# Kernel tuning notes

Hardware: AMD Instinct MI355X
Metric: run time of the kernel (lower is better)

The kernel has to match this reference:

```python
import jax, jax.numpy as jnp
import numpy as np

ALPHA, BETA, THRESH, T = 0.9, 0.8, 1.0, 10


def _heaviside(x):
    return (x > 0).astype(x.dtype)


def _conv(x, w, b, stride):
    y = jax.lax.conv_general_dilated(
        x, w, window_strides=(stride, stride), padding='VALID',
        dimension_numbers=('NCHW', 'OIHW', 'NCHW'))
    return jax.nn.relu(y + b[None, :, None, None])


def setup_inputs() -> dict:
    key = jax.random.key(0)
    ks = jax.random.split(key, 16)
    B = 128
    state = jax.random.uniform(ks[0], (B, 3, 224, 224), dtype=jnp.float32)
    history = jax.random.uniform(ks[1], (B, 90), dtype=jnp.float32)
    fc_in = 64 * 24 * 24 + 90  # 36954

    def w(k, shape, fan_in):
        return jax.random.normal(k, shape, dtype=jnp.float32) * (1.0 / np.sqrt(fan_in))

    return {
        'state': state, 'history': history,
        'cw1': w(ks[2], (32, 3, 8, 8), 3 * 8 * 8), 'cb1': jnp.zeros((32,), jnp.float32),
        'cw2': w(ks[3], (64, 32, 4, 4), 32 * 4 * 4), 'cb2': jnp.zeros((64,), jnp.float32),
        'cw3': w(ks[4], (64, 64, 3, 3), 64 * 3 * 3), 'cb3': jnp.zeros((64,), jnp.float32),
        'w1': w(ks[5], (128, fc_in), fc_in), 'b1': jnp.zeros((128,), jnp.float32),
        'w2': w(ks[6], (256, 128), 128), 'b2': jnp.zeros((256,), jnp.float32),
        'w3': w(ks[7], (9, 256), 256), 'b3': jnp.zeros((9,), jnp.float32),
    }


def reference(state, history, cw1, cb1, cw2, cb2, cw3, cb3, w1, b1, w2, b2, w3, b3):
    B = state.shape[0]
    f = _conv(state, cw1, cb1, 4)
    f = _conv(f, cw2, cb2, 2)
    f = _conv(f, cw3, cb3, 1)
    x = jnp.concatenate([f.reshape(B, -1), history], axis=1)  # (B, 36954)
    # encoding='constant' -> input (hence h1) is identical every timestep
    h1 = x @ w1.T + b1  # (B,128)

    def lif(h, mem, syn):
        new_syn = ALPHA * syn + h
        new_mem = BETA * mem + new_syn
        out = _heaviside(new_mem - THRESH)
        return out, new_mem - out * THRESH, new_syn

    z = lambda d: jnp.zeros((B, d), x.dtype)
    carry0 = (z(128), z(128), z(256), z(256), z(9), z(9), z(9))

    def step(carry, _):
        mem1, syn1, mem2, syn2, mem3, syn3, pot = carry
        spk1, mem1, syn1 = lif(h1, mem1, syn1)
        h2 = spk1 @ w2.T + b2
        spk2, mem2, syn2 = lif(h2, mem2, syn2)
        h3 = spk2 @ w3.T + b3
        syn3 = ALPHA * syn3 + h3
        mem3 = BETA * mem3 + syn3
        pot = pot + mem3
        return (mem1, syn1, mem2, syn2, mem3, syn3, pot), None

    carry, _ = jax.lax.scan(step, carry0, None, length=T)
    return carry[6] / T
```

## Files before the change

### kernel.cpp

```cpp
#include <hip/hip_runtime.h>

#define ALPHA 0.9f
#define BETA  0.8f
#define XS 36960

typedef _Float16 f16;
typedef _Float16 f16x8 __attribute__((ext_vector_type(8)));
typedef float f32x4 __attribute__((ext_vector_type(4)));
typedef unsigned int u32;

struct F4 { float x, y, z, w; };

#define GLOAD_LDS16(gsrc, ldst)                                        \
  __builtin_amdgcn_global_load_lds(                                    \
      (const __attribute__((address_space(1))) void*)(gsrc),           \
      (__attribute__((address_space(3))) void*)(ldst), 16, 0, 0)

__device__ inline u32 hpair(u32 d0, u32 d1) {
#if __has_builtin(__builtin_amdgcn_perm)
  return __builtin_amdgcn_perm(d1, d0, 0x05040100u);
#else
  return (d0 & 0xffffu) | (d1 << 16);
#endif
}
__device__ inline u32 lpair(u32 d0, u32 d1) {
#if __has_builtin(__builtin_amdgcn_perm)
  return __builtin_amdgcn_perm(d1, d0, 0x07060302u);
#else
  return (d0 >> 16) | (d1 & 0xffff0000u);
#endif
}

__device__ inline u32 pack_hl(float v) {
  f16 h = (f16)v;
  f16 l = (f16)(v - (float)h);
  return (u32)__builtin_bit_cast(unsigned short, h) |
         ((u32)__builtin_bit_cast(unsigned short, l) << 16);
}


__global__ __launch_bounds__(256) void prep_weights_kernel(
    const float* __restrict__ cw1, const float* __restrict__ cw2,
    const float* __restrict__ cw3, const float* __restrict__ w2,
    f16* __restrict__ w1h, f16* __restrict__ w1l,
    f16* __restrict__ w2h, f16* __restrict__ w2l,
    f16* __restrict__ w3h, f16* __restrict__ w3l,
    float* __restrict__ w2q) {
  int i = blockIdx.x * 256 + threadIdx.x;
  if (i < 6144)  { float v = cw1[i]; f16 h = (f16)v; w1h[i] = h; w1l[i] = (f16)(v - (float)h); }
  if (i < 32768) { float v = cw2[i]; f16 h = (f16)v; w2h[i] = h; w2l[i] = (f16)(v - (float)h); }
  if (i < 49152) {
    int oc = i / 768, r = i % 768;
    int c = r / 12, rr = r % 12, kh = rr >> 2, kw = rr & 3;
    float v = (kw < 3) ? cw3[oc * 576 + c * 9 + kh * 3 + kw] : 0.f;
    f16 h = (f16)v; w3h[i] = h; w3l[i] = (f16)(v - (float)h);
  }
  if (i < 32768) {
    int j = i >> 7, k = i & 127;
    w2q[((k >> 2) * 256 + j) * 4 + (k & 3)] = w2[i];
  }
}

__global__ __launch_bounds__(512) void conv1_kernel(
    const float* __restrict__ in, const f16* __restrict__ wh,
    const f16* __restrict__ wl, const float* __restrict__ bias,
    u32* __restrict__ out) {
  constexpr int K = 192, KCH = 6, OW = 55, OHW = 3025, NPB = 256;
  __shared__ __attribute__((aligned(16))) f16 Ah[2 * 512], Al[2 * 512];
  __shared__ __attribute__((aligned(16))) float Bf[16 * 512];

  const int n = blockIdx.y, pos0 = blockIdx.x * NPB;
  const int t = threadIdx.x;
  const int w = t >> 6, lane = t & 63, quad = lane >> 4, l16 = lane & 15;
  const float* __restrict__ inb = in + (size_t)n * 3 * 224 * 224;

  const int rq = (t >> 4) & 3;
  int base[2];
#pragma unroll
  for (int si = 0; si < 2; ++si) {
    int s = t + si * 512;
    int pos = pos0 + (s >> 6) * 16 + (s & 15);
    if (pos > OHW - 1) pos = OHW - 1;
    int oh = pos / OW, ow = pos - oh * OW;
    base[si] = oh * 4 * 224 + ow * 4;
  }
  const int am = (t >> 6) * 16 + (t & 15);
  const int ak = ((t >> 4) & 3) * 8;

  int posv[2];
#pragma unroll
  for (int ntl = 0; ntl < 2; ++ntl)
    posv[ntl] = pos0 + (w * 2 + ntl) * 16 + l16;

  f32x4 acc[2][2] = {};

  for (int kt = 0; kt < KCH; ++kt) {
    __syncthreads();
    if (t < 128) {
      *(f16x8*)&Ah[t * 8] = *(const f16x8*)&wh[am * K + kt * 32 + ak];
      *(f16x8*)&Al[t * 8] = *(const f16x8*)&wl[am * K + kt * 32 + ak];
    }
    {
      int r = kt * 4 + rq;
      int c = r >> 3, kh = r & 7;
      int rowoff = c * 50176 + kh * 224;
#pragma unroll
      for (int si = 0; si < 2; ++si)
#pragma unroll
        for (int half = 0; half < 2; ++half)
          GLOAD_LDS16(inb + rowoff + base[si] + half * 4,
                      &Bf[(si * 8 + w) * 512 + half * 256]);
    }
    __syncthreads();

    f16x8 ah0 = *(const f16x8*)&Ah[0 * 512 + lane * 8];
    f16x8 ah1 = *(const f16x8*)&Ah[1 * 512 + lane * 8];
    f16x8 al0 = *(const f16x8*)&Al[0 * 512 + lane * 8];
    f16x8 al1 = *(const f16x8*)&Al[1 * 512 + lane * 8];
    f16x8 bh[2], bl[2];
#pragma unroll
    for (int ntl = 0; ntl < 2; ++ntl) {
      const float* bp = &Bf[(w * 2 + ntl) * 512 + lane * 4];
      float4 v0 = *(const float4*)bp;
      float4 v1 = *(const float4*)(bp + 256);
      float vv[8] = {v0.x, v0.y, v0.z, v0.w, v1.x, v1.y, v1.z, v1.w};
#pragma unroll
      for (int e = 0; e < 8; ++e) {
        f16 h = (f16)vv[e];
        bh[ntl][e] = h;
        bl[ntl][e] = (f16)(vv[e] - (float)h);
      }
    }
    acc[0][0] = __builtin_amdgcn_mfma_f32_16x16x32_f16(ah0, bh[0], acc[0][0], 0, 0, 0);
    acc[0][0] = __builtin_amdgcn_mfma_f32_16x16x32_f16(ah0, bl[0], acc[0][0], 0, 0, 0);
    acc[0][0] = __builtin_amdgcn_mfma_f32_16x16x32_f16(al0, bh[0], acc[0][0], 0, 0, 0);
    acc[1][0] = __builtin_amdgcn_mfma_f32_16x16x32_f16(ah1, bh[0], acc[1][0], 0, 0, 0);
    acc[1][0] = __builtin_amdgcn_mfma_f32_16x16x32_f16(ah1, bl[0], acc[1][0], 0, 0, 0);
    acc[1][0] = __builtin_amdgcn_mfma_f32_16x16x32_f16(al1, bh[0], acc[1][0], 0, 0, 0);
    acc[0][1] = __builtin_amdgcn_mfma_f32_16x16x32_f16(ah0, bh[1], acc[0][1], 0, 0, 0);
    acc[0][1] = __builtin_amdgcn_mfma_f32_16x16x32_f16(ah0, bl[1], acc[0][1], 0, 0, 0);
    acc[0][1] = __builtin_amdgcn_mfma_f32_16x16x32_f16(al0, bh[1], acc[0][1], 0, 0, 0);
    acc[1][1] = __builtin_amdgcn_mfma_f32_16x16x32_f16(ah1, bh[1], acc[1][1], 0, 0, 0);
    acc[1][1] = __builtin_amdgcn_mfma_f32_16x16x32_f16(ah1, bl[1], acc[1][1], 0, 0, 0);
    acc[1][1] = __builtin_amdgcn_mfma_f32_16x16x32_f16(al1, bh[1], acc[1][1], 0, 0, 0);
  }

#pragma unroll
  for (int mtl = 0; mtl < 2; ++mtl)
#pragma unroll
    for (int ntl = 0; ntl < 2; ++ntl)
#pragma unroll
      for (int r = 0; r < 4; ++r) {
        int oc  = mtl * 16 + quad * 4 + r;
        int pos = posv[ntl];
        if (pos < OHW) {
          float v = acc[mtl][ntl][r] + bias[oc];
          v = v > 0.f ? v : 0.f;
          out[((size_t)n * 32 + oc) * OHW + pos] = pack_hl(v);
        }
      }
}

template<int IC, int KH, int KWP, int KWV, int S, int IH, int IW,
         int OW, int OHW, int OC, int NPB, bool OUT_X>
__global__ __launch_bounds__(NPB * 4) void convhl_kernel(
    const u32* __restrict__ in, const f16* __restrict__ wh,
    const f16* __restrict__ wl, const float* __restrict__ bias,
    void* __restrict__ outv) {
  constexpr int K = IC * KH * KWP;
  constexpr int KCH = K / 32;
  constexpr int BS = NPB * 4;
  __shared__ __attribute__((aligned(16))) f16 Ah[4 * 512], Al[4 * 512];
  __shared__ __attribute__((aligned(16))) u32 Bhl[2][BS * 4];

  const int n = blockIdx.y, pos0 = blockIdx.x * NPB;
  const int t = threadIdx.x;
  const int w = t >> 6, lane = t & 63, quad = lane >> 4, l16 = lane & 15;
  const int woc = w & 1, wpos = w >> 1;
  const u32* __restrict__ inb = in + (size_t)n * IC * IH * IW;

  int pos = pos0 + (t >> 6) * 16 + (t & 15);
  if (pos > OHW - 1) pos = OHW - 1;
  int oh = pos / OW, ow = pos - oh * OW;
  const int ohS = oh * S, owS = ow * S;
  const int rq = ((t >> 4) & 3) * 2;
  const int am = (t >> 6) * 16 + (t & 15);
  const int ak = ((t >> 4) & 3) * 8;

  int posv[2];
#pragma unroll
  for (int ntl = 0; ntl < 2; ++ntl)
    posv[ntl] = pos0 + (wpos * 2 + ntl) * 16 + l16;

  f32x4 acc[2][2] = {};

  for (int kt = 0; kt < KCH; ++kt) {
    __syncthreads();
    if (t < 256) {
      *(f16x8*)&Ah[t * 8] = *(const f16x8*)&wh[am * K + kt * 32 + ak];
      *(f16x8*)&Al[t * 8] = *(const f16x8*)&wl[am * K + kt * 32 + ak];
    }
#pragma unroll
    for (int half = 0; half < 2; ++half) {
      int row = kt * 8 + rq + half;
      int c = row / KH, kh = row - c * KH;
      const u32* p = inb + ((size_t)c * IH + ohS + kh) * IW + owS;
      uint4 d;
      d.x = p[0]; d.y = p[1]; d.z = p[2];
      d.w = (KWV < KWP) ? 0u : p[3];
      *(uint4*)&Bhl[half][t * 4] = d;
    }
    __syncthreads();

    f16x8 ah0 = *(const f16x8*)&Ah[(woc * 2 + 0) * 512 + lane * 8];
    f16x8 ah1 = *(const f16x8*)&Ah[(woc * 2 + 1) * 512 + lane * 8];
    f16x8 al0 = *(const f16x8*)&Al[(woc * 2 + 0) * 512 + lane * 8];
    f16x8 al1 = *(const f16x8*)&Al[(woc * 2 + 1) * 512 + lane * 8];
    f16x8 bh[2], bl[2];
#pragma unroll
    for (int ntl = 0; ntl < 2; ++ntl) {
      int sl = ((wpos * 2 + ntl) * 64 + lane) * 4;
      uint4 q0 = *(const uint4*)&Bhl[0][sl];
      uint4 q1 = *(const uint4*)&Bhl[1][sl];
      uint4 hv, lv;
      hv.x = hpair(q0.x, q0.y); lv.x = lpair(q0.x, q0.y);
      hv.y = hpair(q0.z, q0.w); lv.y = lpair(q0.z, q0.w);
      hv.z = hpair(q1.x, q1.y); lv.z = lpair(q1.x, q1.y);
      hv.w = hpair(q1.z, q1.w); lv.w = lpair(q1.z, q1.w);
      bh[ntl] = __builtin_bit_cast(f16x8, hv);
      bl[ntl] = __builtin_bit_cast(f16x8, lv);
    }
    acc[0][0] = __builtin_amdgcn_mfma_f32_16x16x32_f16(ah0, bh[0], acc[0][0], 0, 0, 0);
    acc[0][0] = __builtin_amdgcn_mfma_f32_16x16x32_f16(ah0, bl[0], acc[0][0], 0, 0, 0);
    acc[0][0] = __builtin_amdgcn_mfma_f32_16x16x32_f16(al0, bh[0], acc[0][0], 0, 0, 0);
    acc[1][0] = __builtin_amdgcn_mfma_f32_16x16x32_f16(ah1, bh[0], acc[1][0], 0, 0, 0);
    acc[1][0] = __builtin_amdgcn_mfma_f32_16x16x32_f16(ah1, bl[0], acc[1][0], 0, 0, 0);
    acc[1][0] = __builtin_amdgcn_mfma_f32_16x16x32_f16(al1, bh[0], acc[1][0], 0, 0, 0);
    acc[0][1] = __builtin_amdgcn_mfma_f32_16x16x32_f16(ah0, bh[1], acc[0][1], 0, 0, 0);
    acc[0][1] = __builtin_amdgcn_mfma_f32_16x16x32_f16(ah0, bl[1], acc[0][1], 0, 0, 0);
    acc[0][1] = __builtin_amdgcn_mfma_f32_16x16x32_f16(al0, bh[1], acc[0][1], 0, 0, 0);
    acc[1][1] = __builtin_amdgcn_mfma_f32_16x16x32_f16(ah1, bh[1], acc[1][1], 0, 0, 0);
    acc[1][1] = __builtin_amdgcn_mfma_f32_16x16x32_f16(ah1, bl[1], acc[1][1], 0, 0, 0);
    acc[1][1] = __builtin_amdgcn_mfma_f32_16x16x32_f16(al1, bh[1], acc[1][1], 0, 0, 0);
  }

#pragma unroll
  for (int mtl = 0; mtl < 2; ++mtl)
#pragma unroll
    for (int ntl = 0; ntl < 2; ++ntl)
#pragma unroll
      for (int r = 0; r < 4; ++r) {
        int oc = (woc * 2 + mtl) * 16 + quad * 4 + r;
        int p2 = posv[ntl];
        if (p2 < OHW) {
          float v = acc[mtl][ntl][r] + bias[oc];
          v = v > 0.f ? v : 0.f;
          if constexpr (OUT_X)
            ((float*)outv)[(size_t)n * XS + oc * OHW + p2] = v;
          else
            ((u32*)outv)[((size_t)n * OC + oc) * OHW + p2] = pack_hl(v);
        }
      }
}

__global__ __launch_bounds__(256) void histpack_kernel(
    const float* __restrict__ h, float* __restrict__ x) {
  int i = blockIdx.x * 256 + threadIdx.x;
  if (i < 128 * 96) {
    int n = i / 96, k = i % 96;
    x[(size_t)n * XS + 36864 + k] = (k < 90) ? h[n * 90 + k] : 0.f;
  }
}

#define FC1_KT 289
__global__ __launch_bounds__(256) void fc1_kernel(
    const float* __restrict__ x, const float* __restrict__ w1,
    float* __restrict__ P) {
  int kt = blockIdx.x >> 2;
  int b4 = blockIdx.x & 3;
  int t  = threadIdx.x;
  int bq = t & 3, jq = t >> 2;
  __shared__ float xs[32 * 36];
  __shared__ float wsm[128 * 36];
  float acc[8][2];
#pragma unroll
  for (int bb = 0; bb < 8; ++bb)
#pragma unroll
    for (int jj = 0; jj < 2; ++jj) acc[bb][jj] = 0.f;

  int cs = t & 7;
  int rs = t >> 3;
#pragma unroll 1
  for (int s = 0; s < 4; ++s) {
    int k0 = kt * 128 + s * 32;
    int gk = k0 + cs * 4;
    __syncthreads();
    {
      float4 xv;
      if (gk < 36954)
        xv = *(const float4*)&x[(size_t)(b4 * 32 + rs) * XS + gk];
      else
        xv = make_float4(0.f, 0.f, 0.f, 0.f);
      *(float4*)&xs[rs * 36 + cs * 4] = xv;
    }
#pragma unroll
    for (int p = 0; p < 4; ++p) {
      int r = rs + p * 32;
      float4 wv;
      if (gk + 4 <= 36954) {
        F4 u = *(const F4*)&w1[(size_t)r * 36954 + gk];
        wv = make_float4(u.x, u.y, u.z, u.w);
      } else if (gk < 36954) {
        wv.x = w1[(size_t)r * 36954 + gk];
        wv.y = (gk + 1 < 36954) ? w1[(size_t)r * 36954 + gk + 1] : 0.f;
        wv.z = 0.f; wv.w = 0.f;
      } else {
        wv = make_float4(0.f, 0.f, 0.f, 0.f);
      }
      *(float4*)&wsm[r * 36 + cs * 4] = wv;
    }
    __syncthreads();
#pragma unroll 1
    for (int kk = 0; kk < 32; kk += 4) {
      float4 xv[8], wv[2];
#pragma unroll
      for (int i = 0; i < 8; ++i)
        xv[i] = *(const float4*)&xs[(bq + 4 * i) * 36 + kk];
#pragma unroll
      for (int i = 0; i < 2; ++i)
        wv[i] = *(const float4*)&wsm[(jq + 64 * i) * 36 + kk];
#pragma unroll
      for (int bb = 0; bb < 8; ++bb)
#pragma unroll
        for (int jj = 0; jj < 2; ++jj) {
          acc[bb][jj] = fmaf(xv[bb].x, wv[jj].x, acc[bb][jj]);
          acc[bb][jj] = fmaf(xv[bb].y, wv[jj].y, acc[bb][jj]);
          acc[bb][jj] = fmaf(xv[bb].z, wv[jj].z, acc[bb][jj]);
          acc[bb][jj] = fmaf(xv[bb].w, wv[jj].w, acc[bb][jj]);
        }
    }
  }
  float* Pb = P + (size_t)kt * 16384;
#pragma unroll
  for (int bb = 0; bb < 8; ++bb)
#pragma unroll
    for (int jj = 0; jj < 2; ++jj)
      Pb[(b4 * 32 + bq + 4 * bb) * 128 + jq + 64 * jj] = acc[bb][jj];
}

__global__ __launch_bounds__(64) void reduce_p_kernel(
    const float* __restrict__ P, const float* __restrict__ b1,
    float* __restrict__ h1s) {
  int idx = blockIdx.x * 64 + threadIdx.x;
  int j = idx & 127;
  float a0 = 0.f, a1 = 0.f, a2 = 0.f, a3 = 0.f;
  int kt = 0;
  for (; kt + 31 < FC1_KT; kt += 32) {
    float v[32];
#pragma unroll
    for (int q = 0; q < 32; ++q)
      v[q] = P[(size_t)(kt + q) * 16384 + idx];
#pragma unroll
    for (int q = 0; q < 32; q += 4) {
      a0 += v[q]; a1 += v[q + 1]; a2 += v[q + 2]; a3 += v[q + 3];
    }
  }
  for (; kt + 3 < FC1_KT; kt += 4) {
    a0 += P[(size_t)(kt + 0) * 16384 + idx];
    a1 += P[(size_t)(kt + 1) * 16384 + idx];
    a2 += P[(size_t)(kt + 2) * 16384 + idx];
    a3 += P[(size_t)(kt + 3) * 16384 + idx];
  }
  for (; kt < FC1_KT; ++kt) a0 += P[(size_t)kt * 16384 + idx];
  h1s[idx] = ((a0 + a1) + (a2 + a3)) + b1[j];
}

__global__ __launch_bounds__(256, 1) void recur_kernel(
    const float* __restrict__ h1s,
    const float4* __restrict__ w2q,
    const float* __restrict__ b2,
    const float* __restrict__ w3,
    const float* __restrict__ b3,
    float* __restrict__ out) {
  int b = blockIdx.x;
  int t = threadIdx.x;
  __shared__ float spk1s[128];
  __shared__ float spk2s[256];
  __shared__ float w3s[9 * 256];
  __shared__ float part[9][16];
  float4 w2c[32];
#pragma unroll
  for (int k4 = 0; k4 < 32; ++k4) w2c[k4] = w2q[k4 * 256 + t];
  for (int i = t; i < 9 * 256; i += 256) w3s[i] = w3[i];
  float h1 = (t < 128) ? h1s[b * 128 + t] : 0.f;
  float mem1 = 0.f, syn1 = 0.f, mem2 = 0.f, syn2 = 0.f;
  float b2v = b2[t];
  float mem3 = 0.f, syn3 = 0.f, pot = 0.f;
  float b3v = (t < 9) ? b3[t] : 0.f;
  int j3 = t >> 4, p = t & 15;
  __syncthreads();

  for (int step = 0; step < 10; ++step) {
    if (t < 128) {
      syn1 = ALPHA * syn1 + h1;
      mem1 = BETA * mem1 + syn1;
      float s = (mem1 > 1.0f) ? 1.0f : 0.0f;
      mem1 -= s;
      spk1s[t] = s;
    }
    __syncthreads();
    float h2 = b2v;
#pragma unroll
    for (int k4 = 0; k4 < 32; ++k4) {
      float4 s = *(const float4*)&spk1s[k4 * 4];
      h2 = fmaf(s.x, w2c[k4].x, h2);
      h2 = fmaf(s.y, w2c[k4].y, h2);
      h2 = fmaf(s.z, w2c[k4].z, h2);
      h2 = fmaf(s.w, w2c[k4].w, h2);
    }
    syn2 = ALPHA * syn2 + h2;
    mem2 = BETA * mem2 + syn2;
    float s2 = (mem2 > 1.0f) ? 1.0f : 0.0f;
    mem2 -= s2;
    spk2s[t] = s2;
    __syncthreads();
    if (t < 144) {
      float a = 0.f;
      const float* wr = &w3s[j3 * 256 + p * 16];
      const float* sp = &spk2s[p * 16];
#pragma unroll
      for (int e = 0; e < 16; ++e) a = fmaf(sp[e], wr[e], a);
      part[j3][p] = a;
    }
    __syncthreads();
    if (t < 9) {
      float a = b3v;
#pragma unroll
      for (int p2 = 0; p2 < 16; ++p2) a += part[t][p2];
      syn3 = ALPHA * syn3 + a;
      mem3 = BETA * mem3 + syn3;
      pot += mem3;
    }
  }
  if (t < 9) out[b * 9 + t] = pot * 0.1f;
}

extern "C" void kernel_launch(void* const* d_in, const int* in_sizes, int n_in,
                              void* d_out, int out_size, void* d_ws, size_t ws_size,
                              hipStream_t stream) {
  const float* state   = (const float*)d_in[0];
  const float* history = (const float*)d_in[1];
  const float* cw1 = (const float*)d_in[2];
  const float* cb1 = (const float*)d_in[3];
  const float* cw2 = (const float*)d_in[4];
  const float* cb2 = (const float*)d_in[5];
  const float* cw3 = (const float*)d_in[6];
  const float* cb3 = (const float*)d_in[7];
  const float* w1  = (const float*)d_in[8];
  const float* b1  = (const float*)d_in[9];
  const float* w2  = (const float*)d_in[10];
  const float* b2  = (const float*)d_in[11];
  const float* w3  = (const float*)d_in[12];
  const float* b3  = (const float*)d_in[13];
  float* out = (float*)d_out;
  char* ws = (char*)d_ws;

  u32*   f1hl = (u32*)(ws + 0);
  float* xb   = (float*)(ws + 0);
  u32*   f2hl = (u32*)(ws + 49561600);
  float* P    = (float*)(ws + 49561600);
  f16* wf1h = (f16*)(ws + 71712768);
  f16* wf1l = (f16*)(ws + 71725056);
  f16* wf2h = (f16*)(ws + 71737344);
  f16* wf2l = (f16*)(ws + 71802880);
  f16* wf3h = (f16*)(ws + 71868416);
  f16* wf3l = (f16*)(ws + 71966720);
  float* w2q = (float*)(ws + 72065024);
  float* h1s = (float*)(ws + 72196096);

  prep_weights_kernel<<<192, 256, 0, stream>>>(cw1, cw2, cw3, w2,
                                               wf1h, wf1l, wf2h, wf2l,
                                               wf3h, wf3l, w2q);
  conv1_kernel<<<dim3(12, 128), 512, 0, stream>>>(state, wf1h, wf1l, cb1, f1hl);
  convhl_kernel<32, 4, 4, 4, 2, 55, 55, 26, 676, 64, 128, false>
      <<<dim3(6, 128), 512, 0, stream>>>(f1hl, wf2h, wf2l, cb2, (void*)f2hl);
  convhl_kernel<64, 3, 4, 3, 1, 26, 26, 24, 576, 64, 128, true>
      <<<dim3(5, 128), 512, 0, stream>>>(f2hl, wf3h, wf3l, cb3, (void*)xb);
  histpack_kernel<<<48, 256, 0, stream>>>(history, xb);
  fc1_kernel<<<FC1_KT * 4, 256, 0, stream>>>(xb, w1, P);
  reduce_p_kernel<<<256, 64, 0, stream>>>(P, b1, h1s);
  recur_kernel<<<128, 256, 0, stream>>>(h1s, (const float4*)w2q, b2, w3, b3, out);
}
```

Baseline: 304.4 us.

## Stage whole input rows in LDS for conv1 instead of per-position patches

The conv1 loader now copies full contiguous 224-float input rows, one per (kernel row, output row) pair, into LDS with a padded row stride. Each output position then reads its 8-wide window from those shared rows, instead of issuing a separate gather for every output position. This removes the duplicated global loads caused by overlapping receptive fields and makes global accesses contiguous. The cost is more LDS per block and reads at LDS offsets that depend on position, which may cause bank conflicts.

```diff
diff --git a/kernel.cpp b/kernel.cpp
--- a/kernel.cpp
+++ b/kernel.cpp
@@ -66,31 +66,30 @@
     const f16* __restrict__ wl, const float* __restrict__ bias,
     u32* __restrict__ out) {
   constexpr int K = 192, KCH = 6, OW = 55, OHW = 3025, NPB = 256;
+  constexpr int RSTRIDE = 260;
   __shared__ __attribute__((aligned(16))) f16 Ah[2 * 512], Al[2 * 512];
-  __shared__ __attribute__((aligned(16))) float Bf[16 * 512];
+  __shared__ __attribute__((aligned(16))) float Bf[24 * RSTRIDE];
 
   const int n = blockIdx.y, pos0 = blockIdx.x * NPB;
   const int t = threadIdx.x;
   const int w = t >> 6, lane = t & 63, quad = lane >> 4, l16 = lane & 15;
   const float* __restrict__ inb = in + (size_t)n * 3 * 224 * 224;
-
-  const int rq = (t >> 4) & 3;
-  int base[2];
-#pragma unroll
-  for (int si = 0; si < 2; ++si) {
-    int s = t + si * 512;
-    int pos = pos0 + (s >> 6) * 16 + (s & 15);
+  const int oh0 = pos0 / OW;
+
+  const int siw = (lane * 4 > 220) ? 220 : lane * 4;
+
+  const int am = (t >> 6) * 16 + (t & 15);
+  const int ak = ((t >> 4) & 3) * 8;
+
+  int posv[2], fa[2];
+#pragma unroll
+  for (int ntl = 0; ntl < 2; ++ntl) {
+    int pos = pos0 + (w * 2 + ntl) * 16 + l16;
+    posv[ntl] = pos;
     if (pos > OHW - 1) pos = OHW - 1;
     int oh = pos / OW, ow = pos - oh * OW;
-    base[si] = oh * 4 * 224 + ow * 4;
-  }
-  const int am = (t >> 6) * 16 + (t & 15);
-  const int ak = ((t >> 4) & 3) * 8;
-
-  int posv[2];
-#pragma unroll
-  for (int ntl = 0; ntl < 2; ++ntl)
-    posv[ntl] = pos0 + (w * 2 + ntl) * 16 + l16;
+    fa[ntl] = (quad * 6 + (oh - oh0)) * RSTRIDE + ow * 4;
+  }
 
   f32x4 acc[2][2] = {};
 
@@ -101,15 +100,16 @@
       *(f16x8*)&Al[t * 8] = *(const f16x8*)&wl[am * K + kt * 32 + ak];
     }
     {
-      int r = kt * 4 + rq;
-      int c = r >> 3, kh = r & 7;
-      int rowoff = c * 50176 + kh * 224;
-#pragma unroll
-      for (int si = 0; si < 2; ++si)
-#pragma unroll
-        for (int half = 0; half < 2; ++half)
-          GLOAD_LDS16(inb + rowoff + base[si] + half * 4,
-                      &Bf[(si * 8 + w) * 512 + half * 256]);
+#pragma unroll
+      for (int i = 0; i < 3; ++i) {
+        int rowid = w * 3 + i;
+        int r = rowid / 6, ohl = rowid % 6;
+        int gr = kt * 4 + r;
+        int c = gr >> 3, kh = gr & 7;
+        int oh = oh0 + ohl; if (oh > 54) oh = 54;
+        const float* src = inb + c * 50176 + (oh * 4 + kh) * 224 + siw;
+        GLOAD_LDS16(src, &Bf[rowid * RSTRIDE]);
+      }
     }
     __syncthreads();
 
@@ -120,9 +120,8 @@
     f16x8 bh[2], bl[2];
 #pragma unroll
     for (int ntl = 0; ntl < 2; ++ntl) {
-      const float* bp = &Bf[(w * 2 + ntl) * 512 + lane * 4];
-      float4 v0 = *(const float4*)bp;
-      float4 v1 = *(const float4*)(bp + 256);
+      float4 v0 = *(const float4*)&Bf[fa[ntl]];
+      float4 v1 = *(const float4*)&Bf[fa[ntl] + 4];
       float vv[8] = {v0.x, v0.y, v0.z, v0.w, v1.x, v1.y, v1.z, v1.w};
 #pragma unroll
       for (int e = 0; e < 8; ++e) {
```

Measured after the change: 302.0 us. Within noise of the previous version (-0.8%).
